# Kernel tuning notes

Measured on AMD Instinct MI355X. Metric: run time of the kernel, lower is better.

Reference implementation:

```python
import jax, jax.numpy as jnp
import numpy as np

K = 3
CINS = [1, 16, 32, 48, 64]
COUTS = [16, 32, 48, 64, 80]
POOL = [True, True, True, False, False]


def _bilinear(x, py, px):
    # x: [B,C,H,W]; py,px: [B,K2,H,W] float sample coords. Zero padding outside.
    B, C, H, W = x.shape
    y0 = jnp.floor(py)
    x0 = jnp.floor(px)
    wy = (py - y0)[:, None]  # [B,1,K2,H,W]
    wx = (px - x0)[:, None]
    y0i = y0.astype(jnp.int32)
    x0i = x0.astype(jnp.int32)
    xf = x.reshape(B, C, H * W)

    def gather(yi, xi):
        valid = (yi >= 0) & (yi < H) & (xi >= 0) & (xi < W)
        yc = jnp.clip(yi, 0, H - 1)
        xc = jnp.clip(xi, 0, W - 1)
        flat = (yc * W + xc).reshape(B, 1, -1)
        v = jnp.take_along_axis(xf, jnp.broadcast_to(flat, (B, C, flat.shape[-1])), axis=2)
        v = v.reshape(B, C, *yi.shape[1:])
        return v * valid[:, None].astype(x.dtype)

    v00 = gather(y0i, x0i)
    v01 = gather(y0i, x0i + 1)
    v10 = gather(y0i + 1, x0i)
    v11 = gather(y0i + 1, x0i + 1)
    return (v00 * (1 - wy) * (1 - wx) + v01 * (1 - wy) * wx
            + v10 * wy * (1 - wx) + v11 * wy * wx)


def _deform_conv(x, woff, boff, w):
    # torchvision DeformConv2d v1: offsets from a regular conv, layout [B, 2*K*K, H, W]
    # with (dy, dx) pairs per kernel tap; stride=1, pad=1, dilation=1.
    B, C, H, W = x.shape
    off = jax.lax.conv_general_dilated(
        x, woff, (1, 1), ((1, 1), (1, 1)),
        dimension_numbers=('NCHW', 'OIHW', 'NCHW')) + boff[None, :, None, None]
    off = off.reshape(B, K * K, 2, H, W)
    ky, kx = jnp.meshgrid(jnp.arange(K), jnp.arange(K), indexing='ij')
    # sample position: p = (h - pad + ky + dy, w - pad + kx + dx)
    py = off[:, :, 0] + (jnp.arange(H, dtype=x.dtype)[None, None, :, None] - 1.0) \
        + ky.reshape(-1).astype(x.dtype)[None, :, None, None]
    px = off[:, :, 1] + (jnp.arange(W, dtype=x.dtype)[None, None, None, :] - 1.0) \
        + kx.reshape(-1).astype(x.dtype)[None, :, None, None]
    samp = _bilinear(x, py, px)  # [B,C,K2,H,W]
    return jnp.einsum('bckhw,ock->bohw', samp, w.reshape(w.shape[0], C, K * K))


def _bn_lrelu(x, g, b):
    # BatchNorm2d training-mode forward (batch stats, biased var, eps=1e-5) + LeakyReLU(0.01)
    m = x.mean((0, 2, 3), keepdims=True)
    v = ((x - m) ** 2).mean((0, 2, 3), keepdims=True)
    y = g[None, :, None, None] * (x - m) * jax.lax.rsqrt(v + 1e-5) + b[None, :, None, None]
    return jnp.where(y > 0, y, 0.01 * y)


def _pool(x):
    return jax.lax.reduce_window(x, -jnp.inf, jax.lax.max, (1, 1, 2, 2), (1, 1, 2, 2), 'VALID')


def _forward(x, params):
    for i, pool in enumerate(POOL):
        woff, boff, w, g, b = params[i]
        x = _bn_lrelu(_deform_conv(x, woff, boff, w), g, b)
        if pool:
            x = _pool(x)
    return x


def setup_inputs() -> dict:
    key = jax.random.key(0)
    ks = jax.random.split(key, 8)
    inp = {"x": jax.random.normal(ks[0], (8, 1, 128, 1024), jnp.float32)}
    for i, (ci, co) in enumerate(zip(CINS, COUTS)):
        k1, k2, k3, k4, k5 = jax.random.split(ks[i + 1], 5)
        inp[f"woff{i}"] = jax.random.normal(k1, (2 * K * K, ci, K, K), jnp.float32) * 0.05
        inp[f"boff{i}"] = jax.random.normal(k2, (2 * K * K,), jnp.float32) * 0.01
        inp[f"w{i}"] = jax.random.normal(k3, (co, ci, K, K), jnp.float32) / np.float32(np.sqrt(ci * K * K))
        inp[f"g{i}"] = jnp.ones((co,), jnp.float32) + 0.1 * jax.random.normal(k4, (co,), jnp.float32)
        inp[f"b{i}"] = 0.1 * jax.random.normal(k5, (co,), jnp.float32)
    return inp


def reference(x, woff0, boff0, w0, g0, b0, woff1, boff1, w1, g1, b1,
              woff2, boff2, w2, g2, b2, woff3, boff3, w3, g3, b3,
              woff4, boff4, w4, g4, b4):
    params = [(woff0, boff0, w0, g0, b0), (woff1, boff1, w1, g1, b1),
              (woff2, boff2, w2, g2, b2), (woff3, boff3, w3, g3, b3),
              (woff4, boff4, w4, g4, b4)]
    return _forward(x, params)
```

## Files before the change

### kernel.cpp

```cpp
#include <hip/hip_runtime.h>
#include <math.h>

#define TPB 256


#define OWM0 0
#define OWM1 144
#define OWM2 4752
#define OWM3 18576
#define OWM4 46224
#define OWO0 92304
#define OWO1 92484
#define OWO2 95940
#define OWO3 102852
#define OWO4 113220
#define PACK_FLOATS 131072

struct PackSrc { const float* p[10]; };

__global__ void pack_weights(PackSrc s, float* __restrict__ dst) {
  int seg = blockIdx.y;
  int idx = blockIdx.x * TPB + threadIdx.x;
  int CI, CO, ow;
  if (seg < 5) {
    if (seg == 0)      { CI = 1;  CO = 16; ow = OWM0; }
    else if (seg == 1) { CI = 16; CO = 32; ow = OWM1; }
    else if (seg == 2) { CI = 32; CO = 48; ow = OWM2; }
    else if (seg == 3) { CI = 48; CO = 64; ow = OWM3; }
    else               { CI = 64; CO = 80; ow = OWM4; }
    int n = 9 * CI * CO;
    if (idx >= n) return;
    int o = idx % CO, rest = idx / CO;
    int c = rest % CI, k = rest / CI;
    dst[ow + idx] = s.p[seg][((size_t)o * CI + c) * 9 + k];
  } else if (seg == 5) {
    if (idx >= 180) return;
    int j = idx % 20, t = idx / 20;
    dst[OWO0 + idx] = (j < 18) ? s.p[5][j * 9 + t] : 0.f;
  } else {
    if (seg == 6)      { CI = 16; ow = OWO1; }
    else if (seg == 7) { CI = 32; ow = OWO2; }
    else if (seg == 8) { CI = 48; ow = OWO3; }
    else               { CI = 64; ow = OWO4; }
    int n = 3 * CI * 9 * 8;
    if (idx >= n) return;
    int u = idx % 8, r = idx / 8;
    int t = r % 9, c = (r / 9) % CI, jg = r / (9 * CI);
    dst[ow + idx] = (u < 6) ? s.p[seg][((size_t)(jg * 6 + u) * CI + c) * 9 + t] : 0.f;
  }
}

__device__ __forceinline__ int xcd_swz(int bid, int nwg) {
  return (bid & 7) * (nwg >> 3) + (bid >> 3);
}

__global__ __launch_bounds__(TPB) void dfc_fused0(
    const float* __restrict__ x, const float* __restrict__ woP,
    const float* __restrict__ boff, const float* __restrict__ wmP,
    float* __restrict__ out, int B, int H, int W) {
  const int idx = xcd_swz(blockIdx.x, gridDim.x) * TPB + threadIdx.x;
  const int HW = H * W;
  const int w = idx % W;
  const int h = (idx / W) % H;
  const int b = idx / HW;
  const float* xp = x + (size_t)b * HW;

  float xv[9];
#pragma unroll
  for (int t = 0; t < 9; t++) {
    int yy = h - 1 + t / 3, xx = w - 1 + t % 3;
    xv[t] = (yy >= 0 && yy < H && xx >= 0 && xx < W) ? xp[yy * W + xx] : 0.f;
  }

  float offv[18];
#pragma unroll
  for (int j = 0; j < 18; j++) offv[j] = boff[j];
#pragma unroll
  for (int t = 0; t < 9; t++) {
    const float* wr = &woP[t * 20];
#pragma unroll
    for (int j = 0; j < 18; j++) offv[j] = fmaf(xv[t], wr[j], offv[j]);
  }

  float acc[16];
#pragma unroll
  for (int o = 0; o < 16; o++) acc[o] = 0.f;

#pragma unroll
  for (int k = 0; k < 9; k++) {
    float py = (float)(h - 1 + k / 3) + offv[2 * k];
    float px = (float)(w - 1 + k % 3) + offv[2 * k + 1];
    float fy = floorf(py), fx = floorf(px);
    float wy = py - fy, wx = px - fx;
    int y0 = (int)fy, x0 = (int)fx;
    int y1 = y0 + 1, x1 = x0 + 1;
    bool vy0 = (y0 >= 0) & (y0 < H), vy1 = (y1 >= 0) & (y1 < H);
    bool vx0 = (x0 >= 0) & (x0 < W), vx1 = (x1 >= 0) & (x1 < W);
    int yc0 = min(max(y0, 0), H - 1), yc1 = min(max(y1, 0), H - 1);
    int xc0 = min(max(x0, 0), W - 1), xc1 = min(max(x1, 0), W - 1);
    float w00 = (vy0 && vx0) ? (1.f - wy) * (1.f - wx) : 0.f;
    float w01 = (vy0 && vx1) ? (1.f - wy) * wx : 0.f;
    float w10 = (vy1 && vx0) ? wy * (1.f - wx) : 0.f;
    float w11 = (vy1 && vx1) ? wy * wx : 0.f;
    float sv = xp[yc0 * W + xc0] * w00 + xp[yc0 * W + xc1] * w01
             + xp[yc1 * W + xc0] * w10 + xp[yc1 * W + xc1] * w11;
    const float* wr = &wmP[k * 16];
#pragma unroll
    for (int o = 0; o < 16; o++) acc[o] = fmaf(sv, wr[o], acc[o]);
  }

  float* op = out + (size_t)b * 16 * HW + h * W + w;
#pragma unroll
  for (int o = 0; o < 16; o++) op[(size_t)o * HW] = acc[o];
}

template<int CI, int TPBK>
__global__ __launch_bounds__(TPBK) void off_conv(
    const float* __restrict__ x, const float* __restrict__ wP,
    const float* __restrict__ boff, float* __restrict__ off,
    int B, int H, int W) {
  const int HW = H * W;
  const int npb = HW / TPBK;
  const int bid = xcd_swz(blockIdx.x, gridDim.x);
  const int pxb = bid % npb;
  const int jg = (bid / npb) % 3;
  const int b = bid / (3 * npb);
  const int px = pxb * TPBK + threadIdx.x;
  const int w = px % W, h = px / W;
  const float* xb = x + (size_t)b * HW * CI;
  const float* wj = wP + (size_t)jg * CI * 9 * 8;

  float acc[6];
#pragma unroll
  for (int u = 0; u < 6; u++) acc[u] = boff[jg * 6 + u];

#pragma unroll 1
  for (int t = 0; t < 9; t++) {
    int yy = h - 1 + t / 3, xx = w - 1 + t % 3;
    bool vld = (yy >= 0 && yy < H && xx >= 0 && xx < W);
    int a = vld ? (yy * W + xx) : 0;
    const float* xp = xb + (size_t)a * CI;
    const float* wt = wj + t * 8;
#pragma unroll 4
    for (int cg = 0; cg < CI / 4; cg++) {
      float4 v = *(const float4*)(xp + cg * 4);
      float s0 = vld ? v.x : 0.f;
      float s1 = vld ? v.y : 0.f;
      float s2 = vld ? v.z : 0.f;
      float s3 = vld ? v.w : 0.f;
      const float* w0 = wt + (size_t)cg * 4 * 72;
#pragma unroll
      for (int u = 0; u < 6; u++) {
        float a0 = fmaf(s0, w0[u], acc[u]);
        float a1 = fmaf(s1, w0[72 + u], a0);
        float a2 = fmaf(s2, w0[144 + u], a1);
        acc[u] = fmaf(s3, w0[216 + u], a2);
      }
    }
  }
#pragma unroll
  for (int u = 0; u < 6; u++)
    off[((size_t)b * 18 + jg * 6 + u) * HW + px] = acc[u];
}

template<int CI, int CO, int OGC, int TPBK>
__global__ __launch_bounds__(TPBK) void dfc_og(
    const float* __restrict__ x, const float* __restrict__ off,
    const float* __restrict__ wP, float* __restrict__ out,
    int B, int H, int W) {
  constexpr int COG = CO / OGC;
  const int HW = H * W;
  const int npb = HW / TPBK;
  const int bid = xcd_swz(blockIdx.x, gridDim.x);
  const int og = bid % OGC;
  const int pxb = (bid / OGC) % npb;
  const int b = bid / (OGC * npb);
  const int px = pxb * TPBK + threadIdx.x;
  const int w = px % W, h = px / W;
  const float* xb = x + (size_t)b * HW * CI;

  float offv[18];
  const float* ob = off + (size_t)b * 18 * HW + px;
#pragma unroll
  for (int j = 0; j < 18; j++) offv[j] = ob[(size_t)j * HW];

  float acc[COG];
#pragma unroll
  for (int o = 0; o < COG; o++) acc[o] = 0.f;

#pragma unroll
  for (int k = 0; k < 9; k++) {
    float py = (float)(h - 1 + k / 3) + offv[2 * k];
    float pxx = (float)(w - 1 + k % 3) + offv[2 * k + 1];
    float fy = floorf(py), fx = floorf(pxx);
    float wy = py - fy, wx = pxx - fx;
    int y0 = (int)fy, x0 = (int)fx;
    int y1 = y0 + 1, x1 = x0 + 1;
    bool vy0 = (y0 >= 0) & (y0 < H), vy1 = (y1 >= 0) & (y1 < H);
    bool vx0 = (x0 >= 0) & (x0 < W), vx1 = (x1 >= 0) & (x1 < W);
    int yc0 = min(max(y0, 0), H - 1), yc1 = min(max(y1, 0), H - 1);
    int xc0 = min(max(x0, 0), W - 1), xc1 = min(max(x1, 0), W - 1);
    float w00 = (vy0 && vx0) ? (1.f - wy) * (1.f - wx) : 0.f;
    float w01 = (vy0 && vx1) ? (1.f - wy) * wx : 0.f;
    float w10 = (vy1 && vx0) ? wy * (1.f - wx) : 0.f;
    float w11 = (vy1 && vx1) ? wy * wx : 0.f;
    const float* p00 = xb + (size_t)(yc0 * W + xc0) * CI;
    const float* p01 = xb + (size_t)(yc0 * W + xc1) * CI;
    const float* p10 = xb + (size_t)(yc1 * W + xc0) * CI;
    const float* p11 = xb + (size_t)(yc1 * W + xc1) * CI;
#pragma unroll 2
    for (int cg = 0; cg < CI / 4; cg++) {
      float4 v00 = *(const float4*)(p00 + cg * 4);
      float4 v01 = *(const float4*)(p01 + cg * 4);
      float4 v10 = *(const float4*)(p10 + cg * 4);
      float4 v11 = *(const float4*)(p11 + cg * 4);
      float s0 = v00.x * w00 + v01.x * w01 + v10.x * w10 + v11.x * w11;
      float s1 = v00.y * w00 + v01.y * w01 + v10.y * w10 + v11.y * w11;
      float s2 = v00.z * w00 + v01.z * w01 + v10.z * w10 + v11.z * w11;
      float s3 = v00.w * w00 + v01.w * w01 + v10.w * w10 + v11.w * w11;
      const float* wr = wP + (size_t)(k * CI + cg * 4) * CO + og * COG;
#pragma unroll
      for (int o = 0; o < COG; o++) {
        float a0 = fmaf(s0, wr[o], acc[o]);
        float a1 = fmaf(s1, wr[CO + o], a0);
        float a2 = fmaf(s2, wr[2 * CO + o], a1);
        acc[o] = fmaf(s3, wr[3 * CO + o], a2);
      }
    }
  }

  float* op = out + ((size_t)b * CO + og * COG) * HW + px;
#pragma unroll
  for (int o = 0; o < COG; o++) op[(size_t)o * HW] = acc[o];
}

template<int CI, int CO, int OGB>
__global__ __launch_bounds__(TPB) void dfc_slds(
    const float* __restrict__ x, const float* __restrict__ off,
    const float* __restrict__ wP, float* __restrict__ out,
    int B, int H, int W) {
  constexpr int P = 64;
  constexpr int S = CI / 4;
  constexpr int COG = CO / (4 * OGB);
  constexpr int ROWD = P * 4 + 12;
  constexpr int NT = (P * S) / TPB;

  __shared__ float s_off[18 * P];
  __shared__ float s_samp[S * ROWD];

  const int HW = H * W;
  const int npb = HW / P;
  const int bid = xcd_swz(blockIdx.x, gridDim.x);
  const int ogb = bid % OGB;
  const int pxb = (bid / OGB) % npb;
  const int b = bid / (OGB * npb);
  const int px0 = pxb * P;
  const int tid = threadIdx.x;
  const float* xb = x + (size_t)b * HW * CI;

  for (int t = tid; t < 18 * P; t += TPB) {
    int j = t / P, p = t % P;
    s_off[t] = off[((size_t)b * 18 + j) * HW + px0 + p];
  }

  const int pc = tid & 63;
  const int wid = tid >> 6;
  const int ocb = (ogb * 4 + wid) * COG;

  float acc[COG];
#pragma unroll
  for (int o = 0; o < COG; o++) acc[o] = 0.f;

#pragma unroll 1
  for (int k = 0; k < 9; k++) {
    __syncthreads();
#pragma unroll 1
    for (int tt = 0; tt < NT; tt++) {
      int t = tt * TPB + tid;
      int s = t % S, p = t / S;
      int px = px0 + p;
      int w = px % W, h = px / W;
      float dy = s_off[(2 * k) * P + p];
      float dx = s_off[(2 * k + 1) * P + p];
      float py = (float)(h - 1 + k / 3) + dy;
      float pxx = (float)(w - 1 + k % 3) + dx;
      float fy = floorf(py), fx = floorf(pxx);
      float wy = py - fy, wx = pxx - fx;
      int y0 = (int)fy, x0 = (int)fx;
      int y1 = y0 + 1, x1 = x0 + 1;
      bool vy0 = (y0 >= 0) & (y0 < H), vy1 = (y1 >= 0) & (y1 < H);
      bool vx0 = (x0 >= 0) & (x0 < W), vx1 = (x1 >= 0) & (x1 < W);
      int yc0 = min(max(y0, 0), H - 1), yc1 = min(max(y1, 0), H - 1);
      int xc0 = min(max(x0, 0), W - 1), xc1 = min(max(x1, 0), W - 1);
      float w00 = (vy0 && vx0) ? (1.f - wy) * (1.f - wx) : 0.f;
      float w01 = (vy0 && vx1) ? (1.f - wy) * wx : 0.f;
      float w10 = (vy1 && vx0) ? wy * (1.f - wx) : 0.f;
      float w11 = (vy1 && vx1) ? wy * wx : 0.f;
      float4 v00 = *(const float4*)(xb + (size_t)(yc0 * W + xc0) * CI + s * 4);
      float4 v01 = *(const float4*)(xb + (size_t)(yc0 * W + xc1) * CI + s * 4);
      float4 v10 = *(const float4*)(xb + (size_t)(yc1 * W + xc0) * CI + s * 4);
      float4 v11 = *(const float4*)(xb + (size_t)(yc1 * W + xc1) * CI + s * 4);
      float4 sv;
      sv.x = v00.x * w00 + v01.x * w01 + v10.x * w10 + v11.x * w11;
      sv.y = v00.y * w00 + v01.y * w01 + v10.y * w10 + v11.y * w11;
      sv.z = v00.z * w00 + v01.z * w01 + v10.z * w10 + v11.z * w11;
      sv.w = v00.w * w00 + v01.w * w01 + v10.w * w10 + v11.w * w11;
      *(float4*)&s_samp[s * ROWD + p * 4] = sv;
    }
    __syncthreads();
#pragma unroll
    for (int s = 0; s < S; s++) {
      float4 sv = *(const float4*)&s_samp[s * ROWD + pc * 4];
      float sj0 = sv.x, sj1 = sv.y, sj2 = sv.z, sj3 = sv.w;
      const float* wr = wP + (size_t)(k * CI + s * 4) * CO + ocb;
#pragma unroll
      for (int o = 0; o < COG; o++) {
        float a0 = fmaf(sj0, wr[o], acc[o]);
        float a1 = fmaf(sj1, wr[CO + o], a0);
        float a2 = fmaf(sj2, wr[2 * CO + o], a1);
        acc[o] = fmaf(sj3, wr[3 * CO + o], a2);
      }
    }
  }

  float* op = out + ((size_t)b * CO + ocb) * HW + px0 + pc;
#pragma unroll
  for (int o = 0; o < COG; o++) op[(size_t)o * HW] = acc[o];
}

__global__ void bn_stats_kernel(const float* __restrict__ y,
                                double* __restrict__ st,
                                int B, int C, int HW, int NB) {
  int c = blockIdx.x / NB;
  int sl = blockIdx.x % NB;
  int tid = threadIdx.x;
  double s = 0.0, s2 = 0.0;
  int HW4 = HW >> 2;
  for (int b = 0; b < B; b++) {
    const float4* p = (const float4*)(y + ((size_t)b * C + c) * HW);
    for (int i = sl * TPB + tid; i < HW4; i += NB * TPB) {
      float4 v = p[i];
      s += (double)v.x + (double)v.y + (double)v.z + (double)v.w;
      s2 += (double)v.x * v.x + (double)v.y * v.y
          + (double)v.z * v.z + (double)v.w * v.w;
    }
  }
  __shared__ double rs[TPB], rq[TPB];
  rs[tid] = s;
  rq[tid] = s2;
  __syncthreads();
  for (int o = TPB / 2; o > 0; o >>= 1) {
    if (tid < o) { rs[tid] += rs[tid + o]; rq[tid] += rq[tid + o]; }
    __syncthreads();
  }
  if (tid == 0) {
    atomicAdd(&st[2 * c], rs[0]);
    atomicAdd(&st[2 * c + 1], rq[0]);
  }
}

__global__ void bn_finalize_kernel(const double* __restrict__ st,
                                   const float* __restrict__ g,
                                   const float* __restrict__ bb,
                                   float* __restrict__ ss, int C, int N) {
  int c = threadIdx.x;
  if (c >= C) return;
  double mean = st[2 * c] / N;
  double var = st[2 * c + 1] / N - mean * mean;
  float inv = (float)(1.0 / sqrt(var + 1e-5));
  float sc = g[c] * inv;
  ss[c] = sc;
  ss[C + c] = bb[c] - (float)mean * sc;
}

__global__ void bn_apply_kernel(const float* __restrict__ y,
                                const float* __restrict__ ss,
                                float* __restrict__ out, int C, int HW, int n) {
  int i = blockIdx.x * TPB + threadIdx.x;
  if (i >= n) return;
  int c = (i / HW) % C;
  float v = fmaf(y[i], ss[c], ss[C + c]);
  out[i] = v > 0.f ? v : 0.01f * v;
}

__global__ void bn_apply_nhwc_kernel(const float* __restrict__ y,
                                     const float* __restrict__ ss,
                                     float* __restrict__ out,
                                     int C, int H, int W, int n) {
  int i = blockIdx.x * TPB + threadIdx.x;
  if (i >= n) return;
  int c = i % C;
  int pix = i / C;
  int w = pix % W;
  int h = (pix / W) % H;
  int b = pix / (W * H);
  float v = fmaf(y[(((size_t)b * C + c) * H + h) * W + w], ss[c], ss[C + c]);
  out[i] = v > 0.f ? v : 0.01f * v;
}

__global__ void bn_apply_pool_nhwc_kernel(const float* __restrict__ y,
                                          const float* __restrict__ ss,
                                          float* __restrict__ out,
                                          int C, int H, int W, int n) {
  int i = blockIdx.x * TPB + threadIdx.x;
  if (i >= n) return;
  int Wp = W >> 1, Hp = H >> 1;
  int c = i % C;
  int pw = (i / C) % Wp;
  int ph = (i / C / Wp) % Hp;
  int b = i / (C * Wp * Hp);
  const float* yp = y + (((size_t)b * C + c) * H + 2 * ph) * W + 2 * pw;
  float sc = ss[c], sh = ss[C + c];
  float v0 = fmaf(yp[0], sc, sh);     v0 = v0 > 0.f ? v0 : 0.01f * v0;
  float v1 = fmaf(yp[1], sc, sh);     v1 = v1 > 0.f ? v1 : 0.01f * v1;
  float v2 = fmaf(yp[W], sc, sh);     v2 = v2 > 0.f ? v2 : 0.01f * v2;
  float v3 = fmaf(yp[W + 1], sc, sh); v3 = v3 > 0.f ? v3 : 0.01f * v3;
  out[i] = fmaxf(fmaxf(v0, v1), fmaxf(v2, v3));
}

extern "C" void kernel_launch(void* const* d_in, const int* in_sizes, int n_in,
                              void* d_out, int out_size, void* d_ws, size_t ws_size,
                              hipStream_t stream) {
  const float* x = (const float*)d_in[0];
  const float *woff[5], *boff[5], *wm[5], *g[5], *bb[5];
  for (int i = 0; i < 5; i++) {
    woff[i] = (const float*)d_in[1 + 5 * i + 0];
    boff[i] = (const float*)d_in[1 + 5 * i + 1];
    wm[i]   = (const float*)d_in[1 + 5 * i + 2];
    g[i]    = (const float*)d_in[1 + 5 * i + 3];
    bb[i]   = (const float*)d_in[1 + 5 * i + 4];
  }

  const size_t need =
      (size_t)(16777216 + 4718592 + 4194304 + 2097152 + PACK_FLOATS) * 4 + 6400 + 640;
  if (ws_size < need) return;

  float* conv_buf = (float*)d_ws;
  float* off_buf = conv_buf + 16777216;
  float* xa = off_buf + 4718592;
  float* xb2 = xa + 4194304;
  float* wpk = xb2 + 2097152;
  double* st = (double*)(wpk + PACK_FLOATS);
  float* ss = (float*)(st + 800);

  const int B = 8;

  {
    PackSrc psrc;
    for (int i = 0; i < 5; i++) { psrc.p[i] = wm[i]; psrc.p[5 + i] = woff[i]; }
    pack_weights<<<dim3(180, 10), TPB, 0, stream>>>(psrc, wpk);
    hipMemsetAsync(st, 0, 800 * sizeof(double), stream);
  }

  auto bn_head = [&](const float* ybuf, int C, int H, int W, int NB,
                     const float* gg, const float* bbb, int layer) {
    double* stl = st + 160 * layer;
    bn_stats_kernel<<<C * NB, TPB, 0, stream>>>(ybuf, stl, B, C, H * W, NB);
    bn_finalize_kernel<<<1, TPB, 0, stream>>>(stl, gg, bbb, ss, C, B * H * W);
  };

  {
    const int H = 128, W = 1024;
    dfc_fused0<<<B * H * W / TPB, TPB, 0, stream>>>(
        x, wpk + OWO0, boff[0], wpk + OWM0, conv_buf, B, H, W);
    bn_head(conv_buf, 16, H, W, 32, g[0], bb[0], 0);
    int n = B * 16 * (H / 2) * (W / 2);
    bn_apply_pool_nhwc_kernel<<<n / TPB, TPB, 0, stream>>>(
        conv_buf, ss, xa, 16, H, W, n);
  }
  {
    const int H = 64, W = 512;
    off_conv<16, 256><<<B * 3 * (H * W / 256), 256, 0, stream>>>(
        xa, wpk + OWO1, boff[1], off_buf, B, H, W);
    dfc_og<16, 32, 1, 256><<<B * (H * W / 256), 256, 0, stream>>>(
        xa, off_buf, wpk + OWM1, conv_buf, B, H, W);
    bn_head(conv_buf, 32, H, W, 32, g[1], bb[1], 1);
    int n = B * 32 * (H / 2) * (W / 2);
    bn_apply_pool_nhwc_kernel<<<n / TPB, TPB, 0, stream>>>(
        conv_buf, ss, xb2, 32, H, W, n);
  }
  {
    const int H = 32, W = 256;
    off_conv<32, 256><<<B * 3 * (H * W / 256), 256, 0, stream>>>(
        xb2, wpk + OWO2, boff[2], off_buf, B, H, W);
    dfc_og<32, 48, 2, 256><<<B * (H * W / 256) * 2, 256, 0, stream>>>(
        xb2, off_buf, wpk + OWM2, conv_buf, B, H, W);
    bn_head(conv_buf, 48, H, W, 16, g[2], bb[2], 2);
    int n = B * 48 * (H / 2) * (W / 2);
    bn_apply_pool_nhwc_kernel<<<n / TPB, TPB, 0, stream>>>(
        conv_buf, ss, xa, 48, H, W, n);
  }
  {
    const int H = 16, W = 128;
    off_conv<48, 64><<<B * 3 * (H * W / 64), 64, 0, stream>>>(
        xa, wpk + OWO3, boff[3], off_buf, B, H, W);
    dfc_slds<48, 64, 4><<<B * (H * W / 64) * 4, TPB, 0, stream>>>(
        xa, off_buf, wpk + OWM3, conv_buf, B, H, W);
    bn_head(conv_buf, 64, H, W, 8, g[3], bb[3], 3);
    int n = B * 64 * H * W;
    bn_apply_nhwc_kernel<<<n / TPB, TPB, 0, stream>>>(
        conv_buf, ss, xb2, 64, H, W, n);
  }
  {
    const int H = 16, W = 128;
    off_conv<64, 64><<<B * 3 * (H * W / 64), 64, 0, stream>>>(
        xb2, wpk + OWO4, boff[4], off_buf, B, H, W);
    dfc_slds<64, 80, 4><<<B * (H * W / 64) * 4, TPB, 0, stream>>>(
        xb2, off_buf, wpk + OWM4, conv_buf, B, H, W);
    bn_head(conv_buf, 80, H, W, 8, g[4], bb[4], 4);
    int n = B * 80 * H * W;
    bn_apply_kernel<<<n / TPB, TPB, 0, stream>>>(
        conv_buf, ss, (float*)d_out, 80, H * W, n);
  }
}
```

Before: 543.5 us.

## Replace output-group split deform conv with 8-wave blocks sharing sampled tile

The deform conv for the last two layers used 4 blocks per pixel tile, one per output-channel group, and each block recomputed the same bilinear samples. Now one 512-thread block per pixel tile has 8 waves covering all output channels, so each tile is gathered and interpolated only once. The padded shared-memory row is replaced by an XOR swizzle to avoid bank conflicts. The trade-offs are a quarter as many blocks, which lowers parallelism on small layers, and a partial last iteration when CI=48.

Measured after the change: 572.2 us. +5.3%, slower.

```diff
diff --git a/kernel.cpp b/kernel.cpp
--- a/kernel.cpp
+++ b/kernel.cpp
@@ -234,38 +234,35 @@
   for (int o = 0; o < COG; o++) op[(size_t)o * HW] = acc[o];
 }
 
-template<int CI, int CO, int OGB>
-__global__ __launch_bounds__(TPB) void dfc_slds(
+template<int CI, int CO>
+__global__ __launch_bounds__(512) void dfc_wave8(
     const float* __restrict__ x, const float* __restrict__ off,
     const float* __restrict__ wP, float* __restrict__ out,
     int B, int H, int W) {
   constexpr int P = 64;
   constexpr int S = CI / 4;
-  constexpr int COG = CO / (4 * OGB);
-  constexpr int ROWD = P * 4 + 12;
-  constexpr int NT = (P * S) / TPB;
+  constexpr int COG = CO / 8;
+  constexpr int NT = (P * S + 511) / 512;
 
   __shared__ float s_off[18 * P];
-  __shared__ float s_samp[S * ROWD];
+  __shared__ float s_samp[S * P * 4];
 
   const int HW = H * W;
   const int npb = HW / P;
   const int bid = xcd_swz(blockIdx.x, gridDim.x);
-  const int ogb = bid % OGB;
-  const int pxb = (bid / OGB) % npb;
-  const int b = bid / (OGB * npb);
+  const int pxb = bid % npb;
+  const int b = bid / npb;
   const int px0 = pxb * P;
   const int tid = threadIdx.x;
   const float* xb = x + (size_t)b * HW * CI;
 
-  for (int t = tid; t < 18 * P; t += TPB) {
+  for (int t = tid; t < 18 * P; t += 512) {
     int j = t / P, p = t % P;
     s_off[t] = off[((size_t)b * 18 + j) * HW + px0 + p];
   }
 
-  const int pc = tid & 63;
-  const int wid = tid >> 6;
-  const int ocb = (ogb * 4 + wid) * COG;
+  const int lane = tid & 63;
+  const int og = tid >> 6;
 
   float acc[COG];
 #pragma unroll
@@ -274,56 +271,58 @@
 #pragma unroll 1
   for (int k = 0; k < 9; k++) {
     __syncthreads();
-#pragma unroll 1
+#pragma unroll
     for (int tt = 0; tt < NT; tt++) {
-      int t = tt * TPB + tid;
-      int s = t % S, p = t / S;
-      int px = px0 + p;
-      int w = px % W, h = px / W;
-      float dy = s_off[(2 * k) * P + p];
-      float dx = s_off[(2 * k + 1) * P + p];
-      float py = (float)(h - 1 + k / 3) + dy;
-      float pxx = (float)(w - 1 + k % 3) + dx;
-      float fy = floorf(py), fx = floorf(pxx);
-      float wy = py - fy, wx = pxx - fx;
-      int y0 = (int)fy, x0 = (int)fx;
-      int y1 = y0 + 1, x1 = x0 + 1;
-      bool vy0 = (y0 >= 0) & (y0 < H), vy1 = (y1 >= 0) & (y1 < H);
-      bool vx0 = (x0 >= 0) & (x0 < W), vx1 = (x1 >= 0) & (x1 < W);
-      int yc0 = min(max(y0, 0), H - 1), yc1 = min(max(y1, 0), H - 1);
-      int xc0 = min(max(x0, 0), W - 1), xc1 = min(max(x1, 0), W - 1);
-      float w00 = (vy0 && vx0) ? (1.f - wy) * (1.f - wx) : 0.f;
-      float w01 = (vy0 && vx1) ? (1.f - wy) * wx : 0.f;
-      float w10 = (vy1 && vx0) ? wy * (1.f - wx) : 0.f;
-      float w11 = (vy1 && vx1) ? wy * wx : 0.f;
-      float4 v00 = *(const float4*)(xb + (size_t)(yc0 * W + xc0) * CI + s * 4);
-      float4 v01 = *(const float4*)(xb + (size_t)(yc0 * W + xc1) * CI + s * 4);
-      float4 v10 = *(const float4*)(xb + (size_t)(yc1 * W + xc0) * CI + s * 4);
-      float4 v11 = *(const float4*)(xb + (size_t)(yc1 * W + xc1) * CI + s * 4);
-      float4 sv;
-      sv.x = v00.x * w00 + v01.x * w01 + v10.x * w10 + v11.x * w11;
-      sv.y = v00.y * w00 + v01.y * w01 + v10.y * w10 + v11.y * w11;
-      sv.z = v00.z * w00 + v01.z * w01 + v10.z * w10 + v11.z * w11;
-      sv.w = v00.w * w00 + v01.w * w01 + v10.w * w10 + v11.w * w11;
-      *(float4*)&s_samp[s * ROWD + p * 4] = sv;
+      int t = tt * 512 + tid;
+      if ((P * S) % 512 == 0 || t < P * S) {
+        int s = t % S, p = t / S;
+        int px = px0 + p;
+        int w = px % W, h = px / W;
+        float dy = s_off[(2 * k) * P + p];
+        float dx = s_off[(2 * k + 1) * P + p];
+        float py = (float)(h - 1 + k / 3) + dy;
+        float pxx = (float)(w - 1 + k % 3) + dx;
+        float fy = floorf(py), fx = floorf(pxx);
+        float wy = py - fy, wx = pxx - fx;
+        int y0 = (int)fy, x0 = (int)fx;
+        int y1 = y0 + 1, x1 = x0 + 1;
+        bool vy0 = (y0 >= 0) & (y0 < H), vy1 = (y1 >= 0) & (y1 < H);
+        bool vx0 = (x0 >= 0) & (x0 < W), vx1 = (x1 >= 0) & (x1 < W);
+        int yc0 = min(max(y0, 0), H - 1), yc1 = min(max(y1, 0), H - 1);
+        int xc0 = min(max(x0, 0), W - 1), xc1 = min(max(x1, 0), W - 1);
+        float w00 = (vy0 && vx0) ? (1.f - wy) * (1.f - wx) : 0.f;
+        float w01 = (vy0 && vx1) ? (1.f - wy) * wx : 0.f;
+        float w10 = (vy1 && vx0) ? wy * (1.f - wx) : 0.f;
+        float w11 = (vy1 && vx1) ? wy * wx : 0.f;
+        float4 v00 = *(const float4*)(xb + (size_t)(yc0 * W + xc0) * CI + s * 4);
+        float4 v01 = *(const float4*)(xb + (size_t)(yc0 * W + xc1) * CI + s * 4);
+        float4 v10 = *(const float4*)(xb + (size_t)(yc1 * W + xc0) * CI + s * 4);
+        float4 v11 = *(const float4*)(xb + (size_t)(yc1 * W + xc1) * CI + s * 4);
+        float4 sv;
+        sv.x = v00.x * w00 + v01.x * w01 + v10.x * w10 + v11.x * w11;
+        sv.y = v00.y * w00 + v01.y * w01 + v10.y * w10 + v11.y * w11;
+        sv.z = v00.z * w00 + v01.z * w01 + v10.z * w10 + v11.z * w11;
+        sv.w = v00.w * w00 + v01.w * w01 + v10.w * w10 + v11.w * w11;
+        int u = p ^ (s & 7);
+        *(float4*)&s_samp[(s * P + u) * 4] = sv;
+      }
     }
     __syncthreads();
 #pragma unroll
     for (int s = 0; s < S; s++) {
-      float4 sv = *(const float4*)&s_samp[s * ROWD + pc * 4];
-      float sj0 = sv.x, sj1 = sv.y, sj2 = sv.z, sj3 = sv.w;
-      const float* wr = wP + (size_t)(k * CI + s * 4) * CO + ocb;
+      float4 sv = *(const float4*)&s_samp[(s * P + (lane ^ (s & 7))) * 4];
+      const float* wr = wP + (size_t)(k * CI + s * 4) * CO + og * COG;
 #pragma unroll
       for (int o = 0; o < COG; o++) {
-        float a0 = fmaf(sj0, wr[o], acc[o]);
-        float a1 = fmaf(sj1, wr[CO + o], a0);
-        float a2 = fmaf(sj2, wr[2 * CO + o], a1);
-        acc[o] = fmaf(sj3, wr[3 * CO + o], a2);
+        float a0 = fmaf(sv.x, wr[o], acc[o]);
+        float a1 = fmaf(sv.y, wr[CO + o], a0);
+        float a2 = fmaf(sv.z, wr[2 * CO + o], a1);
+        acc[o] = fmaf(sv.w, wr[3 * CO + o], a2);
       }
     }
   }
 
-  float* op = out + ((size_t)b * CO + ocb) * HW + px0 + pc;
+  float* op = out + ((size_t)b * CO + og * COG) * HW + px0 + lane;
 #pragma unroll
   for (int o = 0; o < COG; o++) op[(size_t)o * HW] = acc[o];
 }
@@ -494,7 +493,7 @@
     const int H = 16, W = 128;
     off_conv<48, 64><<<B * 3 * (H * W / 64), 64, 0, stream>>>(
         xa, wpk + OWO3, boff[3], off_buf, B, H, W);
-    dfc_slds<48, 64, 4><<<B * (H * W / 64) * 4, TPB, 0, stream>>>(
+    dfc_wave8<48, 64><<<B * (H * W / 64), 512, 0, stream>>>(
         xa, off_buf, wpk + OWM3, conv_buf, B, H, W);
     bn_head(conv_buf, 64, H, W, 8, g[3], bb[3], 3);
     int n = B * 64 * H * W;
@@ -505,7 +504,7 @@
     const int H = 16, W = 128;
     off_conv<64, 64><<<B * 3 * (H * W / 64), 64, 0, stream>>>(
         xb2, wpk + OWO4, boff[4], off_buf, B, H, W);
-    dfc_slds<64, 80, 4><<<B * (H * W / 64) * 4, TPB, 0, stream>>>(
+    dfc_wave8<64, 80><<<B * (H * W / 64), 512, 0, stream>>>(
         xb2, off_buf, wpk + OWM4, conv_buf, B, H, W);
     bn_head(conv_buf, 80, H, W, 8, g[4], bb[4], 4);
     int n = B * 80 * H * W;
```
